# Optimization experiments

Hardware: AMD Instinct MI355X
Metric: run time of the kernel (lower is better)

Reference implementation:

```python
import jax, jax.numpy as jnp
import numpy as np
from jax import lax

SF = 2      # scale_factor
K = 5       # up_kernel
G = 1       # up_group
CC = 64     # compressed_channels
EK = 3      # encoder_kernel


def setup_inputs() -> dict:
    key = jax.random.key(0)
    k1, k2, k3, k4, k5 = jax.random.split(key, 5)
    N, C, H, W = 4, 256, 64, 64
    x = jax.random.normal(k1, (N, C, H, W), dtype=jnp.float32)
    # channel compressor: 1x1 conv (CC, C, 1, 1), xavier-ish init
    Wc = jax.random.normal(k2, (CC, C, 1, 1), dtype=jnp.float32) * (1.0 / np.sqrt(C))
    bc = jnp.zeros((CC,), dtype=jnp.float32)
    # content encoder: 3x3 conv -> K*K*G*SF*SF channels
    enc_out = K * K * G * SF * SF
    We = jax.random.normal(k3, (enc_out, CC, EK, EK), dtype=jnp.float32) * (1.0 / np.sqrt(CC * EK * EK))
    be = jnp.zeros((enc_out,), dtype=jnp.float32)
    return {"x": x, "Wc": Wc, "bc": bc, "We": We, "be": be}


def _carafe_forward(x, Wc, bc, We, be):
    N, C, H, W = x.shape
    k2 = K * K
    # channel compressor (1x1 conv)
    comp = lax.conv_general_dilated(x, Wc, (1, 1), 'VALID') + bc[None, :, None, None]
    # content encoder (3x3 conv, padding 1)
    pad_e = (EK - 1) // 2
    m = lax.conv_general_dilated(comp, We, (1, 1), ((pad_e, pad_e), (pad_e, pad_e))) + be[None, :, None, None]
    # pixel shuffle by SF: (N, Cm*SF^2, H, W) -> (N, Cm, H*SF, W*SF)
    Cm = m.shape[1] // (SF * SF)  # == G * K*K
    m = m.reshape(N, Cm, SF, SF, H, W).transpose(0, 1, 4, 2, 5, 3).reshape(N, Cm, H * SF, W * SF)
    # softmax over kernel dimension
    m = jax.nn.softmax(m.reshape(N, G, k2, H * SF, W * SF), axis=2)
    # unfold features into kxk neighborhoods (same padding): (N, C, k2, H, W)
    pad = (K - 1) // 2
    xp = jnp.pad(x, ((0, 0), (0, 0), (pad, pad), (pad, pad)))
    patches = jnp.stack([xp[:, :, i:i + H, j:j + W] for i in range(K) for j in range(K)], axis=2)
    patches = patches.reshape(N, G, C // G, k2, H, W)
    # reassemble: contract over kernel dim BEFORE duplicating to output res.
    # out[n,g,c,h*SF+i,w*SF+j] = sum_k patches[n,g,c,k,h,w] * mask[n,g,k,h*SF+i,w*SF+j]
    mm = m.reshape(N, G, k2, H, SF, W, SF)
    out = jnp.einsum('ngckhw,ngkhiwj->ngchiwj', patches, mm)
    return out.reshape(N, C, H * SF, W * SF)


def reference(x, Wc, bc, We, be):
    return _carafe_forward(x, Wc, bc, We, be)
```

## Files before the change

### kernel.cpp

```cpp
#include <hip/hip_runtime.h>
#include <hip/hip_bf16.h>


#define COMP_F 0
#define WR_F   1115136
#define LOG_F  1179648
#define WS_NEED 11272192ull
#define CSTR 4356

__global__ void k0_wr(const float* __restrict__ We, float* __restrict__ ws) {
    int tid = blockIdx.x * blockDim.x + threadIdx.x;
    if (tid >= 4 * 64 * 9 * 25) return;
    int k  = tid % 25;
    int q  = (tid / 25) % 9;
    int cc = (tid / 225) % 64;
    int ij = tid / 14400;
    ws[WR_F + (((size_t)(ij * 64 + cc) * 9) + q) * 28 + k] =
        We[(size_t)(4 * k + ij) * 576 + cc * 9 + q];
}

__global__ __launch_bounds__(64) void k1_comp(const float* __restrict__ x,
                                              const float* __restrict__ Wc,
                                              const float* __restrict__ bc,
                                              float* __restrict__ ws) {
    int b   = blockIdx.x;
    int pw  = b & 255;
    int ccg = b >> 8;
    int n = pw >> 6, h = pw & 63, w = threadIdx.x;
    int cc0 = ccg * 8;

    float acc[8];
#pragma unroll
    for (int u = 0; u < 8; ++u) acc[u] = 0.f;

    const float* xp = x + (size_t)n * 256 * 4096 + h * 64 + w;
#pragma unroll 4
    for (int c = 0; c < 256; ++c) {
        float xv = xp[(size_t)c * 4096];
#pragma unroll
        for (int u = 0; u < 8; ++u)
            acc[u] += xv * Wc[(cc0 + u) * 256 + c];
    }

    float* compb = ws + COMP_F + (size_t)(n * 64 + cc0) * CSTR;
#pragma unroll
    for (int u = 0; u < 8; ++u) {
        float* cb_ = compb + (size_t)u * CSTR;
        cb_[(h + 1) * 66 + (w + 1)] = acc[u] + bc[cc0 + u];
        if (w < 2) cb_[(h + 1) * 66 + (w ? 65 : 0)] = 0.f;
        if (h == 0)  { cb_[w] = 0.f;           if (w < 2) cb_[64 + w] = 0.f; }
        if (h == 63) { cb_[65 * 66 + w] = 0.f; if (w < 2) cb_[65 * 66 + 64 + w] = 0.f; }
    }
}

template <int K0, int KR>
__device__ void enc_body(const float* __restrict__ compn, const float* __restrict__ wrij,
                         const float* __restrict__ be, float* __restrict__ logits,
                         float* __restrict__ WsL, int n, int th, int tw, int ij) {
    int lane = threadIdx.x;
    int py = lane >> 3, pxx = lane & 7;
    int h = th * 8 + py, w = tw * 8 + pxx;

    float acc[KR];
#pragma unroll
    for (int kk = 0; kk < KR; ++kk) acc[kk] = be[4 * (K0 + kk) + ij];

    for (int cb = 0; cb < 64; cb += 16) {
        for (int p = lane; p < 144; p += 64) {
            int c_ = p / 9, q = p % 9;
            const float* src = wrij + (size_t)(cb + c_) * 252 + q * 28 + K0;
            float* dst = WsL + p * 16;
#pragma unroll
            for (int kk = 0; kk < KR; ++kk) dst[kk] = src[kk];
        }
        __syncthreads();
#pragma unroll 2
        for (int c_ = 0; c_ < 16; ++c_) {
            const float* cp = compn + (size_t)(cb + c_) * CSTR + h * 66 + w;
            float cv[9];
#pragma unroll
            for (int dy = 0; dy < 3; ++dy)
#pragma unroll
                for (int dx = 0; dx < 3; ++dx)
                    cv[dy * 3 + dx] = cp[dy * 66 + dx];
#pragma unroll
            for (int q = 0; q < 9; ++q) {
                float v = cv[q];
                const float* row = WsL + (c_ * 9 + q) * 16;
#pragma unroll
                for (int kk = 0; kk < KR; ++kk) acc[kk] += v * row[kk];
            }
        }
        __syncthreads();
    }

    float* lp = logits + (size_t)(n * 4096 + h * 64 + w) * 100 + ij;
#pragma unroll
    for (int kk = 0; kk < KR; ++kk) lp[4 * (K0 + kk)] = acc[kk];
}

__global__ __launch_bounds__(64) void k2_enc(const float* __restrict__ be,
                                             float* __restrict__ ws) {
    __shared__ float WsL[144 * 16];
    int b    = blockIdx.x;
    int tile = b & 255;
    int ij   = (b >> 8) & 3;
    int kh   = b >> 10;
    int n = tile >> 6, th = (tile >> 3) & 7, tw = tile & 7;

    const float* compn = ws + COMP_F + (size_t)n * 64 * CSTR;
    const float* wrij  = ws + WR_F + (size_t)ij * 64 * 252;
    float* logits = ws + LOG_F;
    if (kh == 0) enc_body<0, 13>(compn, wrij, be, logits, WsL, n, th, tw, ij);
    else         enc_body<13, 12>(compn, wrij, be, logits, WsL, n, th, tw, ij);
}

__global__ __launch_bounds__(256) void k3_out(const float* __restrict__ x,
                                              const float* __restrict__ ws,
                                              float* __restrict__ out) {
    __shared__ float xt[16 * 400];
    int b      = blockIdx.x;
    int tile   = b & 63;
    int cchunk = b >> 6;
    int n = tile >> 4, ty0 = ((tile >> 2) & 3) * 16, tx0 = (tile & 3) * 16;
    int c0 = cchunk * 16;

    const float* xn = x + (size_t)(n * 256 + c0) * 4096;
    for (int e = threadIdx.x; e < 16 * 400; e += 256) {
        int c = e / 400, r = (e % 400) / 20, q = e % 20;
        int hh = ty0 + r - 2, ww = tx0 + q - 2;
        float v = 0.f;
        if (hh >= 0 && hh < 64 && ww >= 0 && ww < 64) v = xn[(size_t)c * 4096 + hh * 64 + ww];
        xt[e] = v;
    }

    int py = threadIdx.x >> 4, pxx = threadIdx.x & 15;
    int h = ty0 + py, w = tx0 + pxx;
    const float* lp = ws + LOG_F + (size_t)(n * 4096 + h * 64 + w) * 100;
    float4 mk[25];
#pragma unroll
    for (int t = 0; t < 25; ++t) mk[t] = ((const float4*)lp)[t];

    float4 mx = mk[0];
#pragma unroll
    for (int t = 1; t < 25; ++t) {
        mx.x = fmaxf(mx.x, mk[t].x); mx.y = fmaxf(mx.y, mk[t].y);
        mx.z = fmaxf(mx.z, mk[t].z); mx.w = fmaxf(mx.w, mk[t].w);
    }
    float4 sm = {0.f, 0.f, 0.f, 0.f};
#pragma unroll
    for (int t = 0; t < 25; ++t) {
        mk[t].x = __expf(mk[t].x - mx.x); sm.x += mk[t].x;
        mk[t].y = __expf(mk[t].y - mx.y); sm.y += mk[t].y;
        mk[t].z = __expf(mk[t].z - mx.z); sm.z += mk[t].z;
        mk[t].w = __expf(mk[t].w - mx.w); sm.w += mk[t].w;
    }
    float4 iv = {1.f / sm.x, 1.f / sm.y, 1.f / sm.z, 1.f / sm.w};
#pragma unroll
    for (int t = 0; t < 25; ++t) {
        mk[t].x *= iv.x; mk[t].y *= iv.y; mk[t].z *= iv.z; mk[t].w *= iv.w;
    }
    __syncthreads();

    for (int c = 0; c < 16; ++c) {
        const float* xc = xt + c * 400 + py * 20 + pxx;
        float a0 = 0.f, a1 = 0.f, a2 = 0.f, a3 = 0.f;
#pragma unroll
        for (int t = 0; t < 25; ++t) {
            float v = xc[(t / 5) * 20 + (t % 5)];
            a0 += v * mk[t].x; a1 += v * mk[t].y;
            a2 += v * mk[t].z; a3 += v * mk[t].w;
        }
        size_t ob = (((size_t)(n * 256 + c0 + c) * 128) + 2 * h) * 128 + 2 * w;
        float2 r0 = {a0, a1}, r1 = {a2, a3};
        *(float2*)(out + ob)       = r0;
        *(float2*)(out + ob + 128) = r1;
    }
}

__global__ __launch_bounds__(256) void k_fused(const float* __restrict__ x,
                                               const float* __restrict__ Wc,
                                               const float* __restrict__ bc,
                                               const float* __restrict__ We,
                                               const float* __restrict__ be,
                                               float* __restrict__ out) {
    __shared__ float compS[64 * 101];
    int n = blockIdx.x >> 6, tile = blockIdx.x & 63;
    int ty0 = (tile >> 3) * 8, tx0 = (tile & 7) * 8;
    const float* xn = x + (size_t)n * 256 * 4096;
    {
        int pa = threadIdx.x & 127;
        int ga = __builtin_amdgcn_readfirstlane(threadIdx.x >> 7);
        bool act = pa < 100;
        int ah = ty0 + pa / 10 - 1, aw = tx0 + pa % 10 - 1;
        bool inb = act && ah >= 0 && ah < 64 && aw >= 0 && aw < 64;
        int xoff = ah * 64 + aw;
        float acc[32];
#pragma unroll
        for (int i = 0; i < 32; ++i) acc[i] = 0.f;
        for (int c = 0; c < 256; ++c) {
            float xv = inb ? xn[(size_t)c * 4096 + xoff] : 0.f;
#pragma unroll
            for (int i = 0; i < 32; ++i) acc[i] += xv * Wc[(ga * 32 + i) * 256 + c];
        }
        if (act)
#pragma unroll
            for (int i = 0; i < 32; ++i) {
                int cc = ga * 32 + i;
                compS[cc * 101 + pa] = inb ? acc[i] + bc[cc] : 0.f;
            }
    }
    __syncthreads();
    int px = threadIdx.x & 63;
    int ij = __builtin_amdgcn_readfirstlane(threadIdx.x >> 6);
    int py = px >> 3, pxx = px & 7;
    int h = ty0 + py, w = tx0 + pxx;
    float m[25];
#pragma unroll
    for (int k = 0; k < 25; ++k) m[k] = be[4 * k + ij];
    for (int cc = 0; cc < 64; ++cc) {
        float cv[9];
#pragma unroll
        for (int dy = 0; dy < 3; ++dy)
#pragma unroll
            for (int dx = 0; dx < 3; ++dx)
                cv[dy * 3 + dx] = compS[cc * 101 + (py + dy) * 10 + (pxx + dx)];
        int base = cc * 9;
#pragma unroll
        for (int k = 0; k < 25; ++k) {
            int eb = (4 * k + ij) * 576 + base;
            float s = 0.f;
#pragma unroll
            for (int qb = 0; qb < 9; ++qb) s += cv[qb] * We[eb + qb];
            m[k] += s;
        }
    }
    float mxv = m[0];
#pragma unroll
    for (int k = 1; k < 25; ++k) mxv = fmaxf(mxv, m[k]);
    float ss = 0.f;
#pragma unroll
    for (int k = 0; k < 25; ++k) { m[k] = __expf(m[k] - mxv); ss += m[k]; }
    float inv = 1.f / ss;
#pragma unroll
    for (int k = 0; k < 25; ++k) m[k] *= inv;
    int offs[25];
    unsigned vm = 0;
#pragma unroll
    for (int t = 0; t < 25; ++t) {
        int hh = h + t / 5 - 2, ww = w + t % 5 - 2;
        bool v = hh >= 0 && hh < 64 && ww >= 0 && ww < 64;
        offs[t] = v ? hh * 64 + ww : 0;
        if (v) vm |= 1u << t;
    }
    size_t outp = ((size_t)n * 256 * 128 + (2 * h + (ij >> 1))) * 128 + (2 * w + (ij & 1));
    for (int c = 0; c < 256; ++c) {
        const float* xc = xn + (size_t)c * 4096;
        float sum = 0.f;
#pragma unroll
        for (int t = 0; t < 25; ++t) {
            float v = ((vm >> t) & 1u) ? xc[offs[t]] : 0.f;
            sum += v * m[t];
        }
        out[outp + (size_t)c * 16384] = sum;
    }
}

extern "C" void kernel_launch(void* const* d_in, const int* in_sizes, int n_in,
                              void* d_out, int out_size, void* d_ws, size_t ws_size,
                              hipStream_t stream) {
    const float* x  = (const float*)d_in[0];
    const float* Wc = (const float*)d_in[1];
    const float* bc = (const float*)d_in[2];
    const float* We = (const float*)d_in[3];
    const float* be = (const float*)d_in[4];
    float* out = (float*)d_out;

    if (ws_size >= WS_NEED && d_ws != nullptr) {
        float* ws = (float*)d_ws;
        hipLaunchKernelGGL(k0_wr,   dim3(225),  dim3(256), 0, stream, We, ws);
        hipLaunchKernelGGL(k1_comp, dim3(2048), dim3(64),  0, stream, x, Wc, bc, ws);
        hipLaunchKernelGGL(k2_enc,  dim3(2048), dim3(64),  0, stream, be, ws);
        hipLaunchKernelGGL(k3_out,  dim3(1024), dim3(256), 0, stream, x, ws, out);
    } else {
        hipLaunchKernelGGL(k_fused, dim3(256),  dim3(256), 0, stream,
                           x, Wc, bc, We, be, out);
    }
}
```

Before: 201.1 us.

## Move softmax into encoder, stage comp tiles in LDS, restructure kernel grids

The encoder kernel now loads an 8x8 (+halo) compressed tile for all 64 channels into shared memory once. Each 256-thread block computes all 25x4 logits for its 64 pixels, with each wave handling one subpixel, and applies softmax there, writing normalized masks in a planar layout. The output kernel then only reads precomputed masks, coalesced per plane, and uses 8x8 tiles with 64 channels per block. Halo zeroing moves into the prep kernel, and the compressor uses 16 output channels per thread in larger blocks. The aim is to remove redundant softmax work and global re-reads, at the cost of fewer, heavier blocks (256) in the encoder and compressor, which may reduce occupancy.

```diff
diff --git a/kernel.cpp b/kernel.cpp
--- a/kernel.cpp
+++ b/kernel.cpp
@@ -4,174 +4,173 @@
 
 #define COMP_F 0
 #define WR_F   1115136
-#define LOG_F  1179648
+#define MSK_F  1179648
 #define WS_NEED 11272192ull
 #define CSTR 4356
 
-__global__ void k0_wr(const float* __restrict__ We, float* __restrict__ ws) {
+__global__ void k0_prep(const float* __restrict__ We, float* __restrict__ ws) {
     int tid = blockIdx.x * blockDim.x + threadIdx.x;
-    if (tid >= 4 * 64 * 9 * 25) return;
-    int k  = tid % 25;
-    int q  = (tid / 25) % 9;
-    int cc = (tid / 225) % 64;
-    int ij = tid / 14400;
-    ws[WR_F + (((size_t)(ij * 64 + cc) * 9) + q) * 28 + k] =
-        We[(size_t)(4 * k + ij) * 576 + cc * 9 + q];
-}
-
-__global__ __launch_bounds__(64) void k1_comp(const float* __restrict__ x,
-                                              const float* __restrict__ Wc,
-                                              const float* __restrict__ bc,
-                                              float* __restrict__ ws) {
-    int b   = blockIdx.x;
-    int pw  = b & 255;
-    int ccg = b >> 8;
-    int n = pw >> 6, h = pw & 63, w = threadIdx.x;
-    int cc0 = ccg * 8;
-
-    float acc[8];
-#pragma unroll
-    for (int u = 0; u < 8; ++u) acc[u] = 0.f;
+    if (tid < 57600) {
+        int k = tid % 25, q = (tid / 25) % 9, cc = (tid / 225) % 64, ij = tid / 14400;
+        ws[WR_F + (((size_t)(ij * 64 + cc) * 9) + q) * 28 + k] =
+            We[(size_t)(4 * k + ij) * 576 + cc * 9 + q];
+    }
+    if (tid < 66560) {
+        int nc = tid / 260, r = tid % 260;
+        int row, col;
+        if (r < 66)       { row = 0;           col = r; }
+        else if (r < 132) { row = 65;          col = r - 66; }
+        else if (r < 196) { row = r - 132 + 1; col = 0; }
+        else              { row = r - 196 + 1; col = 65; }
+        ws[COMP_F + (size_t)nc * CSTR + row * 66 + col] = 0.f;
+    }
+}
+
+__global__ __launch_bounds__(256) void k1_comp(const float* __restrict__ x,
+                                               const float* __restrict__ Wc,
+                                               const float* __restrict__ bc,
+                                               float* __restrict__ ws) {
+    int b = blockIdx.x;
+    int n = b >> 6, h = b & 63;
+    int w   = threadIdx.x & 63;
+    int ccg = threadIdx.x >> 6;
+    int cc0 = ccg * 16;
+
+    float acc[16];
+#pragma unroll
+    for (int u = 0; u < 16; ++u) acc[u] = 0.f;
 
     const float* xp = x + (size_t)n * 256 * 4096 + h * 64 + w;
-#pragma unroll 4
+#pragma unroll 8
     for (int c = 0; c < 256; ++c) {
         float xv = xp[(size_t)c * 4096];
 #pragma unroll
-        for (int u = 0; u < 8; ++u)
+        for (int u = 0; u < 16; ++u)
             acc[u] += xv * Wc[(cc0 + u) * 256 + c];
     }
-
-    float* compb = ws + COMP_F + (size_t)(n * 64 + cc0) * CSTR;
-#pragma unroll
-    for (int u = 0; u < 8; ++u) {
-        float* cb_ = compb + (size_t)u * CSTR;
-        cb_[(h + 1) * 66 + (w + 1)] = acc[u] + bc[cc0 + u];
-        if (w < 2) cb_[(h + 1) * 66 + (w ? 65 : 0)] = 0.f;
-        if (h == 0)  { cb_[w] = 0.f;           if (w < 2) cb_[64 + w] = 0.f; }
-        if (h == 63) { cb_[65 * 66 + w] = 0.f; if (w < 2) cb_[65 * 66 + 64 + w] = 0.f; }
-    }
-}
-
-template <int K0, int KR>
-__device__ void enc_body(const float* __restrict__ compn, const float* __restrict__ wrij,
-                         const float* __restrict__ be, float* __restrict__ logits,
-                         float* __restrict__ WsL, int n, int th, int tw, int ij) {
-    int lane = threadIdx.x;
+#pragma unroll
+    for (int u = 0; u < 16; ++u)
+        ws[COMP_F + (size_t)(n * 64 + cc0 + u) * CSTR + (h + 1) * 66 + (w + 1)]
+            = acc[u] + bc[cc0 + u];
+}
+
+__global__ __launch_bounds__(256) void k2_enc(const float* __restrict__ be,
+                                              float* __restrict__ ws) {
+    __shared__ float compS[6400];
+    __shared__ __align__(16) float wS[4 * 8 * 9 * 28];
+    int b = blockIdx.x;
+    int n = b >> 6, tile = b & 63;
+    int ty0 = (tile >> 3) * 8, tx0 = (tile & 7) * 8;
+    int lane = threadIdx.x & 63, ij = threadIdx.x >> 6;
     int py = lane >> 3, pxx = lane & 7;
-    int h = th * 8 + py, w = tw * 8 + pxx;
-
-    float acc[KR];
-#pragma unroll
-    for (int kk = 0; kk < KR; ++kk) acc[kk] = be[4 * (K0 + kk) + ij];
-
-    for (int cb = 0; cb < 64; cb += 16) {
-        for (int p = lane; p < 144; p += 64) {
-            int c_ = p / 9, q = p % 9;
-            const float* src = wrij + (size_t)(cb + c_) * 252 + q * 28 + K0;
-            float* dst = WsL + p * 16;
-#pragma unroll
-            for (int kk = 0; kk < KR; ++kk) dst[kk] = src[kk];
-        }
+
+    const float* compn = ws + COMP_F + (size_t)n * 64 * CSTR;
+    for (int e = threadIdx.x; e < 6400; e += 256) {
+        int cc = e / 100, p = e % 100;
+        compS[e] = compn[(size_t)cc * CSTR + (ty0 + p / 10) * 66 + (tx0 + p % 10)];
+    }
+
+    float acc[25];
+#pragma unroll
+    for (int k = 0; k < 25; ++k) acc[k] = be[4 * k + ij];
+
+    const float4* WrB = (const float4*)(ws + WR_F);
+    for (int cb = 0; cb < 64; cb += 8) {
         __syncthreads();
-#pragma unroll 2
-        for (int c_ = 0; c_ < 16; ++c_) {
-            const float* cp = compn + (size_t)(cb + c_) * CSTR + h * 66 + w;
+        for (int e = threadIdx.x; e < 2016; e += 256) {
+            int ij_ = e / 504, r = e % 504;
+            ((float4*)wS)[e] = WrB[ij_ * 4032 + cb * 63 + r];
+        }
+        __syncthreads();
+        const float* wij = wS + ij * (8 * 9 * 28);
+#pragma unroll
+        for (int c_ = 0; c_ < 8; ++c_) {
+            int cc = cb + c_;
             float cv[9];
 #pragma unroll
             for (int dy = 0; dy < 3; ++dy)
 #pragma unroll
                 for (int dx = 0; dx < 3; ++dx)
-                    cv[dy * 3 + dx] = cp[dy * 66 + dx];
+                    cv[dy * 3 + dx] = compS[cc * 100 + (py + dy) * 10 + (pxx + dx)];
+            const float* wr = wij + c_ * 9 * 28;
 #pragma unroll
             for (int q = 0; q < 9; ++q) {
                 float v = cv[q];
-                const float* row = WsL + (c_ * 9 + q) * 16;
-#pragma unroll
-                for (int kk = 0; kk < KR; ++kk) acc[kk] += v * row[kk];
+                const float* row = wr + q * 28;
+#pragma unroll
+                for (int kt = 0; kt < 6; ++kt) {
+                    float4 w4 = *(const float4*)(row + 4 * kt);
+                    acc[kt * 4 + 0] += v * w4.x;
+                    acc[kt * 4 + 1] += v * w4.y;
+                    acc[kt * 4 + 2] += v * w4.z;
+                    acc[kt * 4 + 3] += v * w4.w;
+                }
+                acc[24] += v * row[24];
             }
         }
-        __syncthreads();
-    }
-
-    float* lp = logits + (size_t)(n * 4096 + h * 64 + w) * 100 + ij;
-#pragma unroll
-    for (int kk = 0; kk < KR; ++kk) lp[4 * (K0 + kk)] = acc[kk];
-}
-
-__global__ __launch_bounds__(64) void k2_enc(const float* __restrict__ be,
-                                             float* __restrict__ ws) {
-    __shared__ float WsL[144 * 16];
-    int b    = blockIdx.x;
-    int tile = b & 255;
-    int ij   = (b >> 8) & 3;
-    int kh   = b >> 10;
-    int n = tile >> 6, th = (tile >> 3) & 7, tw = tile & 7;
-
-    const float* compn = ws + COMP_F + (size_t)n * 64 * CSTR;
-    const float* wrij  = ws + WR_F + (size_t)ij * 64 * 252;
-    float* logits = ws + LOG_F;
-    if (kh == 0) enc_body<0, 13>(compn, wrij, be, logits, WsL, n, th, tw, ij);
-    else         enc_body<13, 12>(compn, wrij, be, logits, WsL, n, th, tw, ij);
+    }
+
+    float mx = acc[0];
+#pragma unroll
+    for (int k = 1; k < 25; ++k) mx = fmaxf(mx, acc[k]);
+    float s = 0.f;
+#pragma unroll
+    for (int k = 0; k < 25; ++k) { acc[k] = __expf(acc[k] - mx); s += acc[k]; }
+    float inv = 1.f / s;
+    int pix = n * 4096 + (ty0 + py) * 64 + (tx0 + pxx);
+    float* mp = ws + MSK_F;
+#pragma unroll
+    for (int k = 0; k < 25; ++k)
+        mp[(size_t)(ij * 25 + k) * 16384 + pix] = acc[k] * inv;
 }
 
 __global__ __launch_bounds__(256) void k3_out(const float* __restrict__ x,
                                               const float* __restrict__ ws,
                                               float* __restrict__ out) {
-    __shared__ float xt[16 * 400];
-    int b      = blockIdx.x;
-    int tile   = b & 63;
-    int cchunk = b >> 6;
-    int n = tile >> 4, ty0 = ((tile >> 2) & 3) * 16, tx0 = (tile & 3) * 16;
-    int c0 = cchunk * 16;
+    __shared__ float xt[64 * 144];
+    int b = blockIdx.x;
+    int chunk = b >> 8;
+    int t6 = b & 255;
+    int n = t6 >> 6, tile = t6 & 63;
+    int ty0 = (tile >> 3) * 8, tx0 = (tile & 7) * 8;
+    int c0 = chunk * 64;
 
     const float* xn = x + (size_t)(n * 256 + c0) * 4096;
-    for (int e = threadIdx.x; e < 16 * 400; e += 256) {
-        int c = e / 400, r = (e % 400) / 20, q = e % 20;
-        int hh = ty0 + r - 2, ww = tx0 + q - 2;
+    for (int e = threadIdx.x; e < 9216; e += 256) {
+        int c_ = e / 144, p = e % 144;
+        int hh = ty0 + p / 12 - 2, ww = tx0 + p % 12 - 2;
         float v = 0.f;
-        if (hh >= 0 && hh < 64 && ww >= 0 && ww < 64) v = xn[(size_t)c * 4096 + hh * 64 + ww];
+        if (hh >= 0 && hh < 64 && ww >= 0 && ww < 64)
+            v = xn[(size_t)c_ * 4096 + hh * 64 + ww];
         xt[e] = v;
     }
 
-    int py = threadIdx.x >> 4, pxx = threadIdx.x & 15;
-    int h = ty0 + py, w = tx0 + pxx;
-    const float* lp = ws + LOG_F + (size_t)(n * 4096 + h * 64 + w) * 100;
+    int lane = threadIdx.x & 63, cl = threadIdx.x >> 6;
+    int py = lane >> 3, pxx = lane & 7;
+    int pix = n * 4096 + (ty0 + py) * 64 + (tx0 + pxx);
+    const float* mp = ws + MSK_F;
     float4 mk[25];
 #pragma unroll
-    for (int t = 0; t < 25; ++t) mk[t] = ((const float4*)lp)[t];
-
-    float4 mx = mk[0];
-#pragma unroll
-    for (int t = 1; t < 25; ++t) {
-        mx.x = fmaxf(mx.x, mk[t].x); mx.y = fmaxf(mx.y, mk[t].y);
-        mx.z = fmaxf(mx.z, mk[t].z); mx.w = fmaxf(mx.w, mk[t].w);
-    }
-    float4 sm = {0.f, 0.f, 0.f, 0.f};
-#pragma unroll
     for (int t = 0; t < 25; ++t) {
-        mk[t].x = __expf(mk[t].x - mx.x); sm.x += mk[t].x;
-        mk[t].y = __expf(mk[t].y - mx.y); sm.y += mk[t].y;
-        mk[t].z = __expf(mk[t].z - mx.z); sm.z += mk[t].z;
-        mk[t].w = __expf(mk[t].w - mx.w); sm.w += mk[t].w;
-    }
-    float4 iv = {1.f / sm.x, 1.f / sm.y, 1.f / sm.z, 1.f / sm.w};
-#pragma unroll
-    for (int t = 0; t < 25; ++t) {
-        mk[t].x *= iv.x; mk[t].y *= iv.y; mk[t].z *= iv.z; mk[t].w *= iv.w;
+        mk[t].x = mp[(size_t)(t)*16384 + pix];
+        mk[t].y = mp[(size_t)(25 + t) * 16384 + pix];
+        mk[t].z = mp[(size_t)(50 + t) * 16384 + pix];
+        mk[t].w = mp[(size_t)(75 + t) * 16384 + pix];
     }
     __syncthreads();
 
-    for (int c = 0; c < 16; ++c) {
-        const float* xc = xt + c * 400 + py * 20 + pxx;
+    int ce = cl * 16 + 16;
+    for (int c_ = cl * 16; c_ < ce; ++c_) {
+        const float* xc = xt + c_ * 144 + py * 12 + pxx;
         float a0 = 0.f, a1 = 0.f, a2 = 0.f, a3 = 0.f;
 #pragma unroll
         for (int t = 0; t < 25; ++t) {
-            float v = xc[(t / 5) * 20 + (t % 5)];
+            float v = xc[(t / 5) * 12 + (t % 5)];
             a0 += v * mk[t].x; a1 += v * mk[t].y;
             a2 += v * mk[t].z; a3 += v * mk[t].w;
         }
-        size_t ob = (((size_t)(n * 256 + c0 + c) * 128) + 2 * h) * 128 + 2 * w;
+        size_t ob = ((size_t)(n * 256 + c0 + c_) * 128 + 2 * (ty0 + py)) * 128
+                  + 2 * (tx0 + pxx);
         float2 r0 = {a0, a1}, r1 = {a2, a3};
         *(float2*)(out + ob)       = r0;
         *(float2*)(out + ob + 128) = r1;
@@ -278,9 +277,9 @@
 
     if (ws_size >= WS_NEED && d_ws != nullptr) {
         float* ws = (float*)d_ws;
-        hipLaunchKernelGGL(k0_wr,   dim3(225),  dim3(256), 0, stream, We, ws);
-        hipLaunchKernelGGL(k1_comp, dim3(2048), dim3(64),  0, stream, x, Wc, bc, ws);
-        hipLaunchKernelGGL(k2_enc,  dim3(2048), dim3(64),  0, stream, be, ws);
+        hipLaunchKernelGGL(k0_prep, dim3(260),  dim3(256), 0, stream, We, ws);
+        hipLaunchKernelGGL(k1_comp, dim3(256),  dim3(256), 0, stream, x, Wc, bc, ws);
+        hipLaunchKernelGGL(k2_enc,  dim3(256),  dim3(256), 0, stream, be, ws);
         hipLaunchKernelGGL(k3_out,  dim3(1024), dim3(256), 0, stream, x, ws, out);
     } else {
         hipLaunchKernelGGL(k_fused, dim3(256),  dim3(256), 0, stream,
```

After: 292.1 us. 45.2% more time.
